# Optimization experiments

Measured on AMD Instinct MI355X. Metric: run time of the kernel, lower is better.

## Reference

```python
import jax, jax.numpy as jnp
import numpy as np

B, T, D_MODEL, N_HEADS = 2, 2048, 1024, 16
HS = D_MODEL // N_HEADS  # 64


def setup_inputs() -> dict:
    key = jax.random.key(0)
    k1, k2, k3 = jax.random.split(key, 3)
    x = jax.random.normal(k1, (B, T, D_MODEL), dtype=jnp.float32)
    # torch nn.Linear weights: (out_features, in_features)
    W_qkv = jax.random.normal(k2, (3 * D_MODEL, D_MODEL), dtype=jnp.float32) * (D_MODEL ** -0.5)
    W_out = jax.random.normal(k3, (D_MODEL, D_MODEL), dtype=jnp.float32) * (D_MODEL ** -0.5)
    return {"x": x, "W_qkv": W_qkv, "W_out": W_out}


def reference(x, W_qkv, W_out):
    Bx, Tx, Dm = x.shape
    nH, Hs = N_HEADS, HS
    # qkv projection: (B, T, 3*D) -> split heads -> (B, 3*nH, T, Hs) -> chunk
    qkv = x @ W_qkv.T
    qkv = qkv.reshape(Bx, Tx, 3 * nH, Hs).transpose(0, 2, 1, 3)  # B (3nH) T Hs
    q, k, v = qkv[:, :nH], qkv[:, nH:2 * nH], qkv[:, 2 * nH:]
    # q: softmax over head dim, scaled
    q = jax.nn.softmax(q, axis=-1) * (Hs ** -0.5)
    # causal linear attention via cumsum of outer products (non-loop branch)
    k_exp = jnp.exp(k - jnp.max(k, axis=2, keepdims=True))          # B nH T Hs
    k_exp_cumsum = jnp.cumsum(k_exp, axis=2)                        # B nH T Hs
    kv_outer = jnp.einsum('bhtc,bhtd->bhtcd', k_exp, v)             # B nH T Hs Hs
    kv_cumsum = jnp.cumsum(kv_outer, axis=2)                        # B nH T Hs Hs
    kv = kv_cumsum / (k_exp_cumsum[..., None] + 1e-9)
    xo = jnp.einsum('bhtc,bhtcd->bhtd', q, kv)                      # B nH T Hs
    # cat heads: B nH T Hs -> B T (nH Hs)
    xo = xo.transpose(0, 2, 1, 3).reshape(Bx, Tx, Dm)
    return xo @ W_out.T
```

## Files before the change

### kernel.cpp

```cpp
#include <hip/hip_runtime.h>

typedef __bf16 bf16;
typedef __bf16 bf16x8 __attribute__((ext_vector_type(8)));
typedef float  f32x4  __attribute__((ext_vector_type(4)));

#define MFMA16(a, b, c) __builtin_amdgcn_mfma_f32_16x16x32_bf16((a), (b), (c), 0, 0, 0)

#define GLOAD16(gp, lp) __builtin_amdgcn_global_load_lds( \
    (const __attribute__((address_space(1))) void*)(gp),  \
    (__attribute__((address_space(3))) void*)(lp), 16, 0, 0)

#define BAR __builtin_amdgcn_s_barrier()
#define WAITL do { asm volatile("s_waitcnt lgkmcnt(0)" ::: "memory"); \
                   __builtin_amdgcn_sched_barrier(0); } while (0)
#define WAITV6 asm volatile("s_waitcnt vmcnt(6)" ::: "memory")
#define WAITV0 asm volatile("s_waitcnt vmcnt(0)" ::: "memory")

__global__ __launch_bounds__(256) void cvt3_k(const float* __restrict__ x,
                                              const float* __restrict__ wq,
                                              const float* __restrict__ wo,
                                              bf16* __restrict__ xbf,
                                              bf16* __restrict__ wqkv,
                                              bf16* __restrict__ wout) {
    int i = blockIdx.x * 256 + threadIdx.x;
    const float* in; bf16* out; int off;
    if (i < 524288)       { in = x;  out = xbf;  off = i; }
    else if (i < 917504)  { in = wq; out = wqkv; off = i - 524288; }
    else                  { in = wo; out = wout; off = i - 917504; }
    f32x4 a = *(const f32x4*)(in + (size_t)off * 8);
    f32x4 b = *(const f32x4*)(in + (size_t)off * 8 + 4);
    bf16x8 o;
    o[0] = (bf16)a[0]; o[1] = (bf16)a[1]; o[2] = (bf16)a[2]; o[3] = (bf16)a[3];
    o[4] = (bf16)b[0]; o[5] = (bf16)b[1]; o[6] = (bf16)b[2]; o[7] = (bf16)b[3];
    *(bf16x8*)(out + (size_t)off * 8) = o;
}

template <typename CT>
__global__ __launch_bounds__(512, 2) void gemm256(const bf16* __restrict__ A,
                                                  const bf16* __restrict__ B,
                                                  CT* __restrict__ C,
                                                  int M, int N, int K) {
    __shared__ bf16 sA[2][256 * 64];
    __shared__ bf16 sB[2][256 * 64];
    const int tid = threadIdx.x, lane = tid & 63, w = tid >> 6;
    const int wm = w >> 2, wn = w & 3;

    const int nwg = gridDim.x * gridDim.y;
    const int lin = blockIdx.y * gridDim.x + blockIdx.x;
    const int cpx = nwg >> 3;
    const int swzb = (lin & 7) * cpx + (lin >> 3);
    const int row0 = (swzb / gridDim.x) * 256, col0 = (swzb % gridDim.x) * 256;
    const int nt = K >> 6;

    const int sw3   = (lane & 7) * 8;
    const int s0    = (lane >> 4) * 8;
    const int koff0 = s0 ^ sw3;
    const int koff1 = (s0 | 32) ^ sw3;
    const int aoff = (wm * 128 + (lane & 15)) * 64;
    const int boff = (wn * 64  + (lane & 15)) * 64;

    auto stgA = [&](int slot, int t, int i) {
        int c = i * 512 + tid;
        int r = c >> 3;
        int c8 = ((c & 7) * 8) ^ ((r & 7) * 8);
        GLOAD16(A + (size_t)(row0 + r) * K + t * 64 + c8, &sA[slot][c * 8]);
    };
    auto stgB = [&](int slot, int t, int i) {
        int c = i * 512 + tid;
        int r = c >> 3;
        int c8 = ((c & 7) * 8) ^ ((r & 7) * 8);
        GLOAD16(B + (size_t)(col0 + r) * K + t * 64 + c8, &sB[slot][c * 8]);
    };

    f32x4 acc[8][4] = {};

    #pragma unroll
    for (int i = 0; i < 4; ++i) stgA(0, 0, i);
    #pragma unroll
    for (int i = 0; i < 4; ++i) stgB(0, 0, i);
    #pragma unroll
    for (int i = 0; i < 4; ++i) stgA(1, 1, i);
    stgB(1, 1, 0); stgB(1, 1, 1);
    WAITV6;
    BAR;

    for (int j = 0; j < nt; ++j) {
        const int s = j & 1;
        const bf16* sa = sA[s];
        const bf16* sb = sB[s];
        bf16x8 a[4][2], b[4][2];

        #pragma unroll
        for (int mi = 0; mi < 4; ++mi) {
            a[mi][0] = *(const bf16x8*)&sa[aoff + mi * 1024 + koff0];
            a[mi][1] = *(const bf16x8*)&sa[aoff + mi * 1024 + koff1];
        }
        #pragma unroll
        for (int ni = 0; ni < 2; ++ni) {
            b[ni][0] = *(const bf16x8*)&sb[boff + ni * 1024 + koff0];
            b[ni][1] = *(const bf16x8*)&sb[boff + ni * 1024 + koff1];
        }
        if (j + 1 < nt) { stgB(s ^ 1, j + 1, 2); stgB(s ^ 1, j + 1, 3); }
        BAR; WAITL;
        __builtin_amdgcn_s_setprio(1);
        #pragma unroll
        for (int mi = 0; mi < 4; ++mi)
            #pragma unroll
            for (int ni = 0; ni < 2; ++ni) {
                acc[mi][ni] = MFMA16(a[mi][0], b[ni][0], acc[mi][ni]);
                acc[mi][ni] = MFMA16(a[mi][1], b[ni][1], acc[mi][ni]);
            }
        __builtin_amdgcn_s_setprio(0);
        BAR;

        #pragma unroll
        for (int ni = 2; ni < 4; ++ni) {
            b[ni][0] = *(const bf16x8*)&sb[boff + ni * 1024 + koff0];
            b[ni][1] = *(const bf16x8*)&sb[boff + ni * 1024 + koff1];
        }
        BAR; WAITL;
        __builtin_amdgcn_s_setprio(1);
        #pragma unroll
        for (int mi = 0; mi < 4; ++mi)
            #pragma unroll
            for (int ni = 2; ni < 4; ++ni) {
                acc[mi][ni] = MFMA16(a[mi][0], b[ni][0], acc[mi][ni]);
                acc[mi][ni] = MFMA16(a[mi][1], b[ni][1], acc[mi][ni]);
            }
        __builtin_amdgcn_s_setprio(0);
        BAR;

        #pragma unroll
        for (int mi = 0; mi < 4; ++mi) {
            a[mi][0] = *(const bf16x8*)&sa[aoff + (mi + 4) * 1024 + koff0];
            a[mi][1] = *(const bf16x8*)&sa[aoff + (mi + 4) * 1024 + koff1];
        }
        BAR; WAITL;
        __builtin_amdgcn_s_setprio(1);
        #pragma unroll
        for (int mi = 0; mi < 4; ++mi)
            #pragma unroll
            for (int ni = 0; ni < 2; ++ni) {
                acc[mi + 4][ni] = MFMA16(a[mi][0], b[ni][0], acc[mi + 4][ni]);
                acc[mi + 4][ni] = MFMA16(a[mi][1], b[ni][1], acc[mi + 4][ni]);
            }
        __builtin_amdgcn_s_setprio(0);
        BAR;

        if (j + 2 < nt) {
            #pragma unroll
            for (int i = 0; i < 4; ++i) stgA(s, j + 2, i);
            stgB(s, j + 2, 0); stgB(s, j + 2, 1);
            WAITV6;
        } else if (j + 1 < nt) {
            WAITV0;
        }
        BAR; WAITL;
        __builtin_amdgcn_s_setprio(1);
        #pragma unroll
        for (int mi = 0; mi < 4; ++mi)
            #pragma unroll
            for (int ni = 2; ni < 4; ++ni) {
                acc[mi + 4][ni] = MFMA16(a[mi][0], b[ni][0], acc[mi + 4][ni]);
                acc[mi + 4][ni] = MFMA16(a[mi][1], b[ni][1], acc[mi + 4][ni]);
            }
        __builtin_amdgcn_s_setprio(0);
        BAR;
    }

    const int crow = row0 + wm * 128 + (lane >> 4) * 4;
    const int ccol = col0 + wn * 64 + (lane & 15);
    #pragma unroll
    for (int mi = 0; mi < 8; ++mi)
        #pragma unroll
        for (int ni = 0; ni < 4; ++ni)
            #pragma unroll
            for (int r = 0; r < 4; ++r)
                C[(size_t)(crow + mi * 16 + r) * N + ccol + ni * 16] = (CT)acc[mi][ni][r];
}

template <typename CT>
__global__ __launch_bounds__(256) void gemm_nt(const bf16* __restrict__ A,
                                               const bf16* __restrict__ B,
                                               CT* __restrict__ C, int M, int N, int K) {
    __shared__ __align__(16) bf16 As[128 * 64];
    __shared__ __align__(16) bf16 Bs[128 * 64];
    const int tid  = threadIdx.x;
    const int lane = tid & 63;
    const int w    = tid >> 6;
    const int wm   = w >> 1, wn = w & 1;

    const int nwg = gridDim.x * gridDim.y;
    const int lin = blockIdx.y * gridDim.x + blockIdx.x;
    const int cpx = nwg >> 3;
    const int swzb = (lin & 7) * cpx + (lin >> 3);
    const int row0 = (swzb / gridDim.x) * 128, col0 = (swzb % gridDim.x) * 128;

    const int sr   = tid >> 3, sc = (tid & 7) * 8;
    const int sw3   = (lane & 7) * 8;
    const int s0    = (lane >> 4) * 8;
    const int kcs[2] = { s0 ^ sw3, (s0 | 32) ^ sw3 };

    f32x4 acc[4][4] = {};

    for (int k0 = 0; k0 < K; k0 += 64) {
        __syncthreads();
        #pragma unroll
        for (int i = 0; i < 4; ++i) {
            int r = sr + i * 32;
            int c8 = sc ^ ((r & 7) * 8);
            GLOAD16(A + (size_t)(row0 + r) * K + k0 + c8, &As[(i * 256 + tid) * 8]);
            GLOAD16(B + (size_t)(col0 + r) * K + k0 + c8, &Bs[(i * 256 + tid) * 8]);
        }
        __syncthreads();
        #pragma unroll
        for (int kk = 0; kk < 2; ++kk) {
            const int kc = kcs[kk];
            bf16x8 af[4], bfr[4];
            #pragma unroll
            for (int mi = 0; mi < 4; ++mi)
                af[mi] = *(const bf16x8*)&As[(wm * 64 + mi * 16 + (lane & 15)) * 64 + kc];
            #pragma unroll
            for (int ni = 0; ni < 4; ++ni)
                bfr[ni] = *(const bf16x8*)&Bs[(wn * 64 + ni * 16 + (lane & 15)) * 64 + kc];
            #pragma unroll
            for (int mi = 0; mi < 4; ++mi)
                #pragma unroll
                for (int ni = 0; ni < 4; ++ni)
                    acc[mi][ni] = MFMA16(af[mi], bfr[ni], acc[mi][ni]);
        }
    }
    const int crow = row0 + wm * 64 + (lane >> 4) * 4;
    const int ccol = col0 + wn * 64 + (lane & 15);
    #pragma unroll
    for (int mi = 0; mi < 4; ++mi)
        #pragma unroll
        for (int ni = 0; ni < 4; ++ni)
            #pragma unroll
            for (int r = 0; r < 4; ++r)
                C[(size_t)(crow + mi * 16 + r) * N + ccol + ni * 16] = (CT)acc[mi][ni][r];
}

__global__ __launch_bounds__(256) void qsoft_k(bf16* __restrict__ qkv) {
    int tg = blockIdx.x * 256 + threadIdx.x;
    int h = tg & 15, r = tg >> 4;
    bf16* q = qkv + (size_t)r * 3072 + h * 64;
    bf16x8 buf[8];
    float v[64];
    #pragma unroll
    for (int i = 0; i < 8; ++i) buf[i] = *(const bf16x8*)(q + i * 8);
    float m = -3.0e38f;
    #pragma unroll
    for (int i = 0; i < 8; ++i)
        #pragma unroll
        for (int e = 0; e < 8; ++e) { v[i * 8 + e] = (float)buf[i][e]; m = fmaxf(m, v[i * 8 + e]); }
    float s = 0.f;
    #pragma unroll
    for (int i = 0; i < 64; ++i) { v[i] = expf(v[i] - m); s += v[i]; }
    float inv = 0.125f / s;
    #pragma unroll
    for (int i = 0; i < 8; ++i) {
        bf16x8 o;
        #pragma unroll
        for (int e = 0; e < 8; ++e) o[e] = (bf16)(v[i * 8 + e] * inv);
        *(bf16x8*)(q + i * 8) = o;
    }
}

__global__ __launch_bounds__(64) void scanA_k(const bf16* __restrict__ qkv, float* __restrict__ part) {
    int blk = blockIdx.x;
    int bh = blk >> 5, seg = blk & 31;
    int b = bh >> 4, h = bh & 15;
    int c = threadIdx.x;
    const bf16* kb = qkv + (size_t)b * 2048 * 3072 + 1024 + h * 64 + c;
    float s = 0.f;
    for (int t0 = seg * 64; t0 < seg * 64 + 64; t0 += 8) {
        float e[8];
        #pragma unroll
        for (int u = 0; u < 8; ++u) e[u] = (float)kb[(size_t)(t0 + u) * 3072];
        #pragma unroll
        for (int u = 0; u < 8; ++u) s += expf(e[u]);
    }
    part[blk * 64 + c] = s;
}

__global__ __launch_bounds__(64) void scanB_k(bf16* __restrict__ qkv, const float* __restrict__ part) {
    int blk = blockIdx.x;
    int bh = blk >> 5, seg = blk & 31;
    int b = bh >> 4, h = bh & 15;
    int c = threadIdx.x;
    bf16* qb = qkv + (size_t)b * 2048 * 3072 + h * 64 + c;
    bf16* kb = qb + 1024;
    float run = 0.f;
    for (int i = 0; i < seg; ++i) run += part[(bh * 32 + i) * 64 + c];
    for (int t0 = seg * 64; t0 < seg * 64 + 64; t0 += 8) {
        float e[8], qv[8];
        #pragma unroll
        for (int u = 0; u < 8; ++u) e[u] = (float)kb[(size_t)(t0 + u) * 3072];
        #pragma unroll
        for (int u = 0; u < 8; ++u) qv[u] = (float)qb[(size_t)(t0 + u) * 3072];
        #pragma unroll
        for (int u = 0; u < 8; ++u) {
            e[u] = expf(e[u]);
            run += e[u];
            qv[u] = qv[u] / (run + 1e-9f);
        }
        #pragma unroll
        for (int u = 0; u < 8; ++u) {
            qb[(size_t)(t0 + u) * 3072] = (bf16)qv[u];
            kb[(size_t)(t0 + u) * 3072] = (bf16)e[u];
        }
    }
}

__global__ __launch_bounds__(256) void kvchunk_k(const bf16* __restrict__ qkv, float* __restrict__ Wc) {
    __shared__ bf16 KT[64][136];
    __shared__ bf16 VT[64][136];
    const int blk = blockIdx.x, bh = blk >> 4, j = blk & 15;
    const int b = bh >> 4, h = bh & 15;
    const int tid = threadIdx.x, lane = tid & 63, w = tid >> 6;
    const bf16* kbase = qkv + (size_t)(b * 2048 + j * 128) * 3072 + 1024 + h * 64;
    const bf16* vbase = kbase + 1024;

    #pragma unroll
    for (int i = 0; i < 4; ++i) {
        int idx = i * 256 + tid;
        int s = idx >> 3, cg = (idx & 7) * 8;
        bf16x8 k8 = *(const bf16x8*)(kbase + (size_t)s * 3072 + cg);
        bf16x8 v8 = *(const bf16x8*)(vbase + (size_t)s * 3072 + cg);
        #pragma unroll
        for (int e = 0; e < 8; ++e) {
            int d = cg + e;
            int sw2 = s ^ (((d >> 3) & 7) << 3);
            KT[d][sw2] = k8[e];
            VT[d][sw2] = v8[e];
        }
    }
    __syncthreads();

    f32x4 acc[4] = {};
    const int dr = w * 16 + (lane & 15);
    const int swd = ((dr >> 3) & 7) << 3;
    #pragma unroll
    for (int ks = 0; ks < 4; ++ks) {
        const int sc = ks * 32 + (lane >> 4) * 8;
        bf16x8 av = *(const bf16x8*)&VT[dr][sc ^ swd];
        #pragma unroll
        for (int ni = 0; ni < 4; ++ni) {
            int cr = ni * 16 + (lane & 15);
            bf16x8 bk = *(const bf16x8*)&KT[cr][sc ^ (((cr >> 3) & 7) << 3)];
            acc[ni] = MFMA16(av, bk, acc[ni]);
        }
    }
    float* out = Wc + (size_t)blk * 4096;
    const int dw = w * 16 + (lane >> 4) * 4;
    #pragma unroll
    for (int ni = 0; ni < 4; ++ni)
        #pragma unroll
        for (int r = 0; r < 4; ++r)
            out[(dw + r) * 64 + ni * 16 + (lane & 15)] = acc[ni][r];
}

__global__ __launch_bounds__(256) void kvscan_k(const float* __restrict__ Wc, bf16* __restrict__ Wpre) {
    int e = blockIdx.x * 256 + threadIdx.x;
    int bh = e >> 12, off = e & 4095;
    float run = 0.f;
    #pragma unroll
    for (int j = 0; j < 16; ++j) {
        size_t idx = (size_t)(bh * 16 + j) * 4096 + off;
        Wpre[idx] = (bf16)run;
        run += Wc[idx];
    }
}

__global__ __launch_bounds__(256) void attn2_k(const bf16* __restrict__ qkv,
                                               const bf16* __restrict__ Wpre,
                                               bf16* __restrict__ xo) {
    __shared__ bf16 Ks[128][72];
    __shared__ bf16 VTs[64][136];
    __shared__ bf16 Ss[128][136];
    const int bh = blockIdx.y, b = bh >> 4, h = bh & 15;
    const int ti = blockIdx.x, t0 = ti * 128;
    const int tid = threadIdx.x, lane = tid & 63, w = tid >> 6;
    const bf16* qn = qkv + (size_t)b * 2048 * 3072 + h * 64;
    const bf16* ke = qn + 1024;
    const bf16* vv = qn + 2048;

    bf16x8 qf[2][2];
    #pragma unroll
    for (int mi = 0; mi < 2; ++mi)
        #pragma unroll
        for (int kk = 0; kk < 2; ++kk)
            qf[mi][kk] = *(const bf16x8*)(qn + (size_t)(t0 + w * 32 + mi * 16 + (lane & 15)) * 3072
                                          + kk * 32 + (lane >> 4) * 8);
    const bf16* wp = Wpre + (size_t)(bh * 16 + ti) * 4096;
    bf16x8 wf[4][2];
    #pragma unroll
    for (int ni = 0; ni < 4; ++ni)
        #pragma unroll
        for (int kk = 0; kk < 2; ++kk)
            wf[ni][kk] = *(const bf16x8*)(wp + (ni * 16 + (lane & 15)) * 64 + kk * 32 + (lane >> 4) * 8);

    #pragma unroll
    for (int i = 0; i < 4; ++i) {
        int idx = i * 256 + tid;
        int s = idx >> 3, cg = (idx & 7) * 8;
        *(f32x4*)&Ks[s][cg] = *(const f32x4*)(ke + (size_t)(t0 + s) * 3072 + cg);
        bf16x8 v8 = *(const bf16x8*)(vv + (size_t)(t0 + s) * 3072 + cg);
        #pragma unroll
        for (int e = 0; e < 8; ++e) {
            int d = cg + e;
            VTs[d][s ^ (((d >> 3) & 7) << 3)] = v8[e];
        }
    }
    __syncthreads();

    f32x4 accO[2][4] = {};
    #pragma unroll
    for (int kk = 0; kk < 2; ++kk)
        #pragma unroll
        for (int mi = 0; mi < 2; ++mi)
            #pragma unroll
            for (int ni = 0; ni < 4; ++ni)
                accO[mi][ni] = MFMA16(qf[mi][kk], wf[ni][kk], accO[mi][ni]);

    f32x4 accS[2][8] = {};
    #pragma unroll
    for (int kk = 0; kk < 2; ++kk) {
        const int kc = kk * 32 + (lane >> 4) * 8;
        bf16x8 kf[8];
        #pragma unroll
        for (int ni = 0; ni < 8; ++ni) kf[ni] = *(const bf16x8*)&Ks[ni * 16 + (lane & 15)][kc];
        #pragma unroll
        for (int mi = 0; mi < 2; ++mi)
            #pragma unroll
            for (int ni = 0; ni < 8; ++ni)
                accS[mi][ni] = MFMA16(qf[mi][kk], kf[ni], accS[mi][ni]);
    }
    #pragma unroll
    for (int mi = 0; mi < 2; ++mi)
        #pragma unroll
        for (int ni = 0; ni < 8; ++ni) {
            const int tb = w * 32 + mi * 16 + (lane >> 4) * 4;
            const int sb = ni * 16 + (lane & 15);
            #pragma unroll
            for (int r = 0; r < 4; ++r) {
                float sv = accS[mi][ni][r];
                if (sb > tb + r) sv = 0.f;
                Ss[tb + r][sb] = (bf16)sv;
            }
        }
    __syncthreads();

    #pragma unroll
    for (int ks = 0; ks < 4; ++ks) {
        const int kc = ks * 32 + (lane >> 4) * 8;
        bf16x8 sf[2], vf[4];
        #pragma unroll
        for (int mi = 0; mi < 2; ++mi) sf[mi] = *(const bf16x8*)&Ss[w * 32 + mi * 16 + (lane & 15)][kc];
        #pragma unroll
        for (int ni = 0; ni < 4; ++ni) {
            int d = ni * 16 + (lane & 15);
            vf[ni] = *(const bf16x8*)&VTs[d][kc ^ (((d >> 3) & 7) << 3)];
        }
        #pragma unroll
        for (int mi = 0; mi < 2; ++mi)
            #pragma unroll
            for (int ni = 0; ni < 4; ++ni)
                accO[mi][ni] = MFMA16(sf[mi], vf[ni], accO[mi][ni]);
    }

    #pragma unroll
    for (int mi = 0; mi < 2; ++mi)
        #pragma unroll
        for (int ni = 0; ni < 4; ++ni) {
            const int trow = t0 + w * 32 + mi * 16 + (lane >> 4) * 4;
            const int d = ni * 16 + (lane & 15);
            #pragma unroll
            for (int r = 0; r < 4; ++r)
                xo[(size_t)(b * 2048 + trow + r) * 1024 + h * 64 + d] = (bf16)accO[mi][ni][r];
        }
}

extern "C" void kernel_launch(void* const* d_in, const int* in_sizes, int n_in,
                              void* d_out, int out_size, void* d_ws, size_t ws_size,
                              hipStream_t stream) {
    const float* x  = (const float*)d_in[0];
    const float* wq = (const float*)d_in[1];
    const float* wo = (const float*)d_in[2];

    char* ws = (char*)d_ws;
    bf16*  xbf  = (bf16*)(ws);
    float* Wc   = (float*)(ws);
    bf16*  xo   = (bf16*)(ws);
    bf16*  wqkv = (bf16*)(ws + (8u << 20));
    bf16*  Wpre = (bf16*)(ws + (8u << 20));
    bf16*  wout = (bf16*)(ws + (14u << 20));
    bf16*  qkv  = (bf16*)(ws + (16u << 20));
    float* part = (float*)(ws + (40u << 20));

    cvt3_k<<<4096, 256, 0, stream>>>(x, wq, wo, xbf, wqkv, wout);

    gemm256<bf16><<<dim3(12, 16), 512, 0, stream>>>(xbf, wqkv, qkv, 4096, 3072, 1024);

    qsoft_k<<<256, 256, 0, stream>>>(qkv);
    scanA_k<<<1024, 64, 0, stream>>>(qkv, part);
    scanB_k<<<1024, 64, 0, stream>>>(qkv, part);

    kvchunk_k<<<512, 256, 0, stream>>>(qkv, Wc);
    kvscan_k<<<512, 256, 0, stream>>>(Wc, Wpre);
    attn2_k<<<dim3(16, 32), 256, 0, stream>>>(qkv, Wpre, xo);

    gemm_nt<float><<<dim3(8, 32), 256, 0, stream>>>(xo, wout, (float*)d_out, 4096, 1024, 1024);
}
```

Baseline: 124.7 us.

## Software-pipeline LDS fragment loads in GEMM and merge q-softmax with k-exp scan

```diff
diff --git a/kernel.cpp b/kernel.cpp
--- a/kernel.cpp
+++ b/kernel.cpp
@@ -11,10 +11,236 @@
     (__attribute__((address_space(3))) void*)(lp), 16, 0, 0)
 
 #define BAR __builtin_amdgcn_s_barrier()
-#define WAITL do { asm volatile("s_waitcnt lgkmcnt(0)" ::: "memory"); \
-                   __builtin_amdgcn_sched_barrier(0); } while (0)
-#define WAITV6 asm volatile("s_waitcnt vmcnt(6)" ::: "memory")
+#define WAITV8 asm volatile("s_waitcnt vmcnt(8)" ::: "memory")
 #define WAITV0 asm volatile("s_waitcnt vmcnt(0)" ::: "memory")
+
+template <typename CT>
+__global__ __launch_bounds__(512, 2) void gemm256(const bf16* __restrict__ A,
+                                                  const bf16* __restrict__ B,
+                                                  CT* __restrict__ C,
+                                                  int M, int N, int K) {
+    __shared__ bf16 sA[2][256 * 64];
+    __shared__ bf16 sB[2][256 * 64];
+    const int tid = threadIdx.x, lane = tid & 63, w = tid >> 6;
+    const int wm = w >> 2, wn = w & 3;
+
+    const int nwg = gridDim.x * gridDim.y;
+    const int lin = blockIdx.y * gridDim.x + blockIdx.x;
+    const int cpx = nwg >> 3;
+    const int swzb = (lin & 7) * cpx + (lin >> 3);
+    const int row0 = (swzb / gridDim.x) * 256, col0 = (swzb % gridDim.x) * 256;
+    const int nt = K >> 6;
+
+    const int sw3   = (lane & 7) * 8;
+    const int s0    = (lane >> 4) * 8;
+    const int koff0 = s0 ^ sw3;
+    const int koff1 = (s0 | 32) ^ sw3;
+    const int aoff = (wm * 128 + (lane & 15)) * 64;
+    const int boff = (wn * 64  + (lane & 15)) * 64;
+
+    auto stgA = [&](int slot, int t, int i) {
+        int c = i * 512 + tid;
+        int r = c >> 3;
+        int c8 = ((c & 7) * 8) ^ ((r & 7) * 8);
+        GLOAD16(A + (size_t)(row0 + r) * K + t * 64 + c8, &sA[slot][c * 8]);
+    };
+    auto stgB = [&](int slot, int t, int i) {
+        int c = i * 512 + tid;
+        int r = c >> 3;
+        int c8 = ((c & 7) * 8) ^ ((r & 7) * 8);
+        GLOAD16(B + (size_t)(col0 + r) * K + t * 64 + c8, &sB[slot][c * 8]);
+    };
+
+    f32x4 acc[8][4] = {};
+    bf16x8 a[4][2], b[2][2], a2[4][2], b2[2][2];
+
+    #pragma unroll
+    for (int i = 0; i < 4; ++i) stgA(0, 0, i);
+    #pragma unroll
+    for (int i = 0; i < 4; ++i) stgB(0, 0, i);
+    #pragma unroll
+    for (int i = 0; i < 4; ++i) stgA(1, 1, i);
+    #pragma unroll
+    for (int i = 0; i < 4; ++i) stgB(1, 1, i);
+    WAITV8;
+    BAR;
+    {
+        const bf16* sa = sA[0];
+        const bf16* sb = sB[0];
+        #pragma unroll
+        for (int mi = 0; mi < 4; ++mi) {
+            a[mi][0] = *(const bf16x8*)&sa[aoff + mi * 1024 + koff0];
+            a[mi][1] = *(const bf16x8*)&sa[aoff + mi * 1024 + koff1];
+        }
+        #pragma unroll
+        for (int ni = 0; ni < 2; ++ni) {
+            b[ni][0] = *(const bf16x8*)&sb[boff + ni * 1024 + koff0];
+            b[ni][1] = *(const bf16x8*)&sb[boff + ni * 1024 + koff1];
+        }
+    }
+
+    for (int j = 0; j < nt; ++j) {
+        const int s = j & 1;
+        const bf16* sa = sA[s];
+        const bf16* sb = sB[s];
+        const bf16* san = sA[s ^ 1];
+        const bf16* sbn = sB[s ^ 1];
+
+        #pragma unroll
+        for (int ni = 0; ni < 2; ++ni) {
+            b2[ni][0] = *(const bf16x8*)&sb[boff + (ni + 2) * 1024 + koff0];
+            b2[ni][1] = *(const bf16x8*)&sb[boff + (ni + 2) * 1024 + koff1];
+        }
+        BAR;
+        __builtin_amdgcn_s_setprio(1);
+        #pragma unroll
+        for (int mi = 0; mi < 4; ++mi)
+            #pragma unroll
+            for (int ni = 0; ni < 2; ++ni) {
+                acc[mi][ni] = MFMA16(a[mi][0], b[ni][0], acc[mi][ni]);
+                acc[mi][ni] = MFMA16(a[mi][1], b[ni][1], acc[mi][ni]);
+            }
+        __builtin_amdgcn_s_setprio(0);
+        BAR;
+
+        #pragma unroll
+        for (int mi = 0; mi < 4; ++mi) {
+            a2[mi][0] = *(const bf16x8*)&sa[aoff + (mi + 4) * 1024 + koff0];
+            a2[mi][1] = *(const bf16x8*)&sa[aoff + (mi + 4) * 1024 + koff1];
+        }
+        BAR;
+        __builtin_amdgcn_s_setprio(1);
+        #pragma unroll
+        for (int mi = 0; mi < 4; ++mi)
+            #pragma unroll
+            for (int ni = 0; ni < 2; ++ni) {
+                acc[mi][ni + 2] = MFMA16(a[mi][0], b2[ni][0], acc[mi][ni + 2]);
+                acc[mi][ni + 2] = MFMA16(a[mi][1], b2[ni][1], acc[mi][ni + 2]);
+            }
+        __builtin_amdgcn_s_setprio(0);
+        BAR;
+
+        if (j + 2 < nt) {
+            #pragma unroll
+            for (int i = 0; i < 4; ++i) stgB(s, j + 2, i);
+        }
+        BAR;
+        __builtin_amdgcn_s_setprio(1);
+        #pragma unroll
+        for (int mi = 0; mi < 4; ++mi)
+            #pragma unroll
+            for (int ni = 0; ni < 2; ++ni) {
+                acc[mi + 4][ni] = MFMA16(a2[mi][0], b[ni][0], acc[mi + 4][ni]);
+                acc[mi + 4][ni] = MFMA16(a2[mi][1], b[ni][1], acc[mi + 4][ni]);
+            }
+        __builtin_amdgcn_s_setprio(0);
+        BAR;
+
+        if (j + 2 < nt) {
+            #pragma unroll
+            for (int i = 0; i < 4; ++i) stgA(s, j + 2, i);
+            WAITV8;
+        } else if (j + 1 < nt) {
+            WAITV0;
+        }
+        BAR;
+        if (j + 1 < nt) {
+            #pragma unroll
+            for (int mi = 0; mi < 4; ++mi) {
+                a[mi][0] = *(const bf16x8*)&san[aoff + mi * 1024 + koff0];
+                a[mi][1] = *(const bf16x8*)&san[aoff + mi * 1024 + koff1];
+            }
+            #pragma unroll
+            for (int ni = 0; ni < 2; ++ni) {
+                b[ni][0] = *(const bf16x8*)&sbn[boff + ni * 1024 + koff0];
+                b[ni][1] = *(const bf16x8*)&sbn[boff + ni * 1024 + koff1];
+            }
+            __builtin_amdgcn_sched_barrier(0);
+        }
+        __builtin_amdgcn_s_setprio(1);
+        #pragma unroll
+        for (int mi = 0; mi < 4; ++mi)
+            #pragma unroll
+            for (int ni = 0; ni < 2; ++ni) {
+                acc[mi + 4][ni + 2] = MFMA16(a2[mi][0], b2[ni][0], acc[mi + 4][ni + 2]);
+                acc[mi + 4][ni + 2] = MFMA16(a2[mi][1], b2[ni][1], acc[mi + 4][ni + 2]);
+            }
+        __builtin_amdgcn_s_setprio(0);
+        BAR;
+    }
+
+    const int crow = row0 + wm * 128 + (lane >> 4) * 4;
+    const int ccol = col0 + wn * 64 + (lane & 15);
+    #pragma unroll
+    for (int mi = 0; mi < 8; ++mi)
+        #pragma unroll
+        for (int ni = 0; ni < 4; ++ni)
+            #pragma unroll
+            for (int r = 0; r < 4; ++r)
+                C[(size_t)(crow + mi * 16 + r) * N + ccol + ni * 16] = (CT)acc[mi][ni][r];
+}
+
+template <typename CT>
+__global__ __launch_bounds__(256) void gemm_nt(const bf16* __restrict__ A,
+                                               const bf16* __restrict__ B,
+                                               CT* __restrict__ C, int M, int N, int K) {
+    __shared__ __align__(16) bf16 As[128 * 64];
+    __shared__ __align__(16) bf16 Bs[128 * 64];
+    const int tid  = threadIdx.x;
+    const int lane = tid & 63;
+    const int w    = tid >> 6;
+    const int wm   = w >> 1, wn = w & 1;
+
+    const int nwg = gridDim.x * gridDim.y;
+    const int lin = blockIdx.y * gridDim.x + blockIdx.x;
+    const int cpx = nwg >> 3;
+    const int swzb = (lin & 7) * cpx + (lin >> 3);
+    const int row0 = (swzb / gridDim.x) * 128, col0 = (swzb % gridDim.x) * 128;
+
+    const int sr   = tid >> 3, sc = (tid & 7) * 8;
+    const int sw3   = (lane & 7) * 8;
+    const int s0    = (lane >> 4) * 8;
+    const int kcs[2] = { s0 ^ sw3, (s0 | 32) ^ sw3 };
+
+    f32x4 acc[4][4] = {};
+
+    for (int k0 = 0; k0 < K; k0 += 64) {
+        __syncthreads();
+        #pragma unroll
+        for (int i = 0; i < 4; ++i) {
+            int r = sr + i * 32;
+            int c8 = sc ^ ((r & 7) * 8);
+            GLOAD16(A + (size_t)(row0 + r) * K + k0 + c8, &As[(i * 256 + tid) * 8]);
+            GLOAD16(B + (size_t)(col0 + r) * K + k0 + c8, &Bs[(i * 256 + tid) * 8]);
+        }
+        __syncthreads();
+        #pragma unroll
+        for (int kk = 0; kk < 2; ++kk) {
+            const int kc = kcs[kk];
+            bf16x8 af[4], bfr[4];
+            #pragma unroll
+            for (int mi = 0; mi < 4; ++mi)
+                af[mi] = *(const bf16x8*)&As[(wm * 64 + mi * 16 + (lane & 15)) * 64 + kc];
+            #pragma unroll
+            for (int ni = 0; ni < 4; ++ni)
+                bfr[ni] = *(const bf16x8*)&Bs[(wn * 64 + ni * 16 + (lane & 15)) * 64 + kc];
+            #pragma unroll
+            for (int mi = 0; mi < 4; ++mi)
+                #pragma unroll
+                for (int ni = 0; ni < 4; ++ni)
+                    acc[mi][ni] = MFMA16(af[mi], bfr[ni], acc[mi][ni]);
+        }
+    }
+    const int crow = row0 + wm * 64 + (lane >> 4) * 4;
+    const int ccol = col0 + wn * 64 + (lane & 15);
+    #pragma unroll
+    for (int mi = 0; mi < 4; ++mi)
+        #pragma unroll
+        for (int ni = 0; ni < 4; ++ni)
+            #pragma unroll
+            for (int r = 0; r < 4; ++r)
+                C[(size_t)(crow + mi * 16 + r) * N + ccol + ni * 16] = (CT)acc[mi][ni][r];
+}
 
 __global__ __launch_bounds__(256) void cvt3_k(const float* __restrict__ x,
                                               const float* __restrict__ wq,
@@ -35,253 +261,47 @@
     *(bf16x8*)(out + (size_t)off * 8) = o;
 }
 
-template <typename CT>
-__global__ __launch_bounds__(512, 2) void gemm256(const bf16* __restrict__ A,
-                                                  const bf16* __restrict__ B,
-                                                  CT* __restrict__ C,
-                                                  int M, int N, int K) {
-    __shared__ bf16 sA[2][256 * 64];
-    __shared__ bf16 sB[2][256 * 64];
-    const int tid = threadIdx.x, lane = tid & 63, w = tid >> 6;
-    const int wm = w >> 2, wn = w & 3;
-
-    const int nwg = gridDim.x * gridDim.y;
-    const int lin = blockIdx.y * gridDim.x + blockIdx.x;
-    const int cpx = nwg >> 3;
-    const int swzb = (lin & 7) * cpx + (lin >> 3);
-    const int row0 = (swzb / gridDim.x) * 256, col0 = (swzb % gridDim.x) * 256;
-    const int nt = K >> 6;
-
-    const int sw3   = (lane & 7) * 8;
-    const int s0    = (lane >> 4) * 8;
-    const int koff0 = s0 ^ sw3;
-    const int koff1 = (s0 | 32) ^ sw3;
-    const int aoff = (wm * 128 + (lane & 15)) * 64;
-    const int boff = (wn * 64  + (lane & 15)) * 64;
-
-    auto stgA = [&](int slot, int t, int i) {
-        int c = i * 512 + tid;
-        int r = c >> 3;
-        int c8 = ((c & 7) * 8) ^ ((r & 7) * 8);
-        GLOAD16(A + (size_t)(row0 + r) * K + t * 64 + c8, &sA[slot][c * 8]);
-    };
-    auto stgB = [&](int slot, int t, int i) {
-        int c = i * 512 + tid;
-        int r = c >> 3;
-        int c8 = ((c & 7) * 8) ^ ((r & 7) * 8);
-        GLOAD16(B + (size_t)(col0 + r) * K + t * 64 + c8, &sB[slot][c * 8]);
-    };
-
-    f32x4 acc[8][4] = {};
-
-    #pragma unroll
-    for (int i = 0; i < 4; ++i) stgA(0, 0, i);
-    #pragma unroll
-    for (int i = 0; i < 4; ++i) stgB(0, 0, i);
-    #pragma unroll
-    for (int i = 0; i < 4; ++i) stgA(1, 1, i);
-    stgB(1, 1, 0); stgB(1, 1, 1);
-    WAITV6;
-    BAR;
-
-    for (int j = 0; j < nt; ++j) {
-        const int s = j & 1;
-        const bf16* sa = sA[s];
-        const bf16* sb = sB[s];
-        bf16x8 a[4][2], b[4][2];
-
-        #pragma unroll
-        for (int mi = 0; mi < 4; ++mi) {
-            a[mi][0] = *(const bf16x8*)&sa[aoff + mi * 1024 + koff0];
-            a[mi][1] = *(const bf16x8*)&sa[aoff + mi * 1024 + koff1];
-        }
-        #pragma unroll
-        for (int ni = 0; ni < 2; ++ni) {
-            b[ni][0] = *(const bf16x8*)&sb[boff + ni * 1024 + koff0];
-            b[ni][1] = *(const bf16x8*)&sb[boff + ni * 1024 + koff1];
-        }
-        if (j + 1 < nt) { stgB(s ^ 1, j + 1, 2); stgB(s ^ 1, j + 1, 3); }
-        BAR; WAITL;
-        __builtin_amdgcn_s_setprio(1);
-        #pragma unroll
-        for (int mi = 0; mi < 4; ++mi)
-            #pragma unroll
-            for (int ni = 0; ni < 2; ++ni) {
-                acc[mi][ni] = MFMA16(a[mi][0], b[ni][0], acc[mi][ni]);
-                acc[mi][ni] = MFMA16(a[mi][1], b[ni][1], acc[mi][ni]);
-            }
-        __builtin_amdgcn_s_setprio(0);
-        BAR;
-
-        #pragma unroll
-        for (int ni = 2; ni < 4; ++ni) {
-            b[ni][0] = *(const bf16x8*)&sb[boff + ni * 1024 + koff0];
-            b[ni][1] = *(const bf16x8*)&sb[boff + ni * 1024 + koff1];
-        }
-        BAR; WAITL;
-        __builtin_amdgcn_s_setprio(1);
-        #pragma unroll
-        for (int mi = 0; mi < 4; ++mi)
-            #pragma unroll
-            for (int ni = 2; ni < 4; ++ni) {
-                acc[mi][ni] = MFMA16(a[mi][0], b[ni][0], acc[mi][ni]);
-                acc[mi][ni] = MFMA16(a[mi][1], b[ni][1], acc[mi][ni]);
-            }
-        __builtin_amdgcn_s_setprio(0);
-        BAR;
-
-        #pragma unroll
-        for (int mi = 0; mi < 4; ++mi) {
-            a[mi][0] = *(const bf16x8*)&sa[aoff + (mi + 4) * 1024 + koff0];
-            a[mi][1] = *(const bf16x8*)&sa[aoff + (mi + 4) * 1024 + koff1];
-        }
-        BAR; WAITL;
-        __builtin_amdgcn_s_setprio(1);
-        #pragma unroll
-        for (int mi = 0; mi < 4; ++mi)
-            #pragma unroll
-            for (int ni = 0; ni < 2; ++ni) {
-                acc[mi + 4][ni] = MFMA16(a[mi][0], b[ni][0], acc[mi + 4][ni]);
-                acc[mi + 4][ni] = MFMA16(a[mi][1], b[ni][1], acc[mi + 4][ni]);
-            }
-        __builtin_amdgcn_s_setprio(0);
-        BAR;
-
-        if (j + 2 < nt) {
-            #pragma unroll
-            for (int i = 0; i < 4; ++i) stgA(s, j + 2, i);
-            stgB(s, j + 2, 0); stgB(s, j + 2, 1);
-            WAITV6;
-        } else if (j + 1 < nt) {
-            WAITV0;
-        }
-        BAR; WAITL;
-        __builtin_amdgcn_s_setprio(1);
-        #pragma unroll
-        for (int mi = 0; mi < 4; ++mi)
-            #pragma unroll
-            for (int ni = 2; ni < 4; ++ni) {
-                acc[mi + 4][ni] = MFMA16(a[mi][0], b[ni][0], acc[mi + 4][ni]);
-                acc[mi + 4][ni] = MFMA16(a[mi][1], b[ni][1], acc[mi + 4][ni]);
-            }
-        __builtin_amdgcn_s_setprio(0);
-        BAR;
-    }
-
-    const int crow = row0 + wm * 128 + (lane >> 4) * 4;
-    const int ccol = col0 + wn * 64 + (lane & 15);
-    #pragma unroll
-    for (int mi = 0; mi < 8; ++mi)
-        #pragma unroll
-        for (int ni = 0; ni < 4; ++ni)
-            #pragma unroll
-            for (int r = 0; r < 4; ++r)
-                C[(size_t)(crow + mi * 16 + r) * N + ccol + ni * 16] = (CT)acc[mi][ni][r];
-}
-
-template <typename CT>
-__global__ __launch_bounds__(256) void gemm_nt(const bf16* __restrict__ A,
-                                               const bf16* __restrict__ B,
-                                               CT* __restrict__ C, int M, int N, int K) {
-    __shared__ __align__(16) bf16 As[128 * 64];
-    __shared__ __align__(16) bf16 Bs[128 * 64];
-    const int tid  = threadIdx.x;
-    const int lane = tid & 63;
-    const int w    = tid >> 6;
-    const int wm   = w >> 1, wn = w & 1;
-
-    const int nwg = gridDim.x * gridDim.y;
-    const int lin = blockIdx.y * gridDim.x + blockIdx.x;
-    const int cpx = nwg >> 3;
-    const int swzb = (lin & 7) * cpx + (lin >> 3);
-    const int row0 = (swzb / gridDim.x) * 128, col0 = (swzb % gridDim.x) * 128;
-
-    const int sr   = tid >> 3, sc = (tid & 7) * 8;
-    const int sw3   = (lane & 7) * 8;
-    const int s0    = (lane >> 4) * 8;
-    const int kcs[2] = { s0 ^ sw3, (s0 | 32) ^ sw3 };
-
-    f32x4 acc[4][4] = {};
-
-    for (int k0 = 0; k0 < K; k0 += 64) {
-        __syncthreads();
-        #pragma unroll
-        for (int i = 0; i < 4; ++i) {
-            int r = sr + i * 32;
-            int c8 = sc ^ ((r & 7) * 8);
-            GLOAD16(A + (size_t)(row0 + r) * K + k0 + c8, &As[(i * 256 + tid) * 8]);
-            GLOAD16(B + (size_t)(col0 + r) * K + k0 + c8, &Bs[(i * 256 + tid) * 8]);
-        }
-        __syncthreads();
-        #pragma unroll
-        for (int kk = 0; kk < 2; ++kk) {
-            const int kc = kcs[kk];
-            bf16x8 af[4], bfr[4];
-            #pragma unroll
-            for (int mi = 0; mi < 4; ++mi)
-                af[mi] = *(const bf16x8*)&As[(wm * 64 + mi * 16 + (lane & 15)) * 64 + kc];
-            #pragma unroll
-            for (int ni = 0; ni < 4; ++ni)
-                bfr[ni] = *(const bf16x8*)&Bs[(wn * 64 + ni * 16 + (lane & 15)) * 64 + kc];
-            #pragma unroll
-            for (int mi = 0; mi < 4; ++mi)
-                #pragma unroll
-                for (int ni = 0; ni < 4; ++ni)
-                    acc[mi][ni] = MFMA16(af[mi], bfr[ni], acc[mi][ni]);
-        }
-    }
-    const int crow = row0 + wm * 64 + (lane >> 4) * 4;
-    const int ccol = col0 + wn * 64 + (lane & 15);
-    #pragma unroll
-    for (int mi = 0; mi < 4; ++mi)
-        #pragma unroll
-        for (int ni = 0; ni < 4; ++ni)
-            #pragma unroll
-            for (int r = 0; r < 4; ++r)
-                C[(size_t)(crow + mi * 16 + r) * N + ccol + ni * 16] = (CT)acc[mi][ni][r];
-}
-
-__global__ __launch_bounds__(256) void qsoft_k(bf16* __restrict__ qkv) {
-    int tg = blockIdx.x * 256 + threadIdx.x;
-    int h = tg & 15, r = tg >> 4;
-    bf16* q = qkv + (size_t)r * 3072 + h * 64;
-    bf16x8 buf[8];
-    float v[64];
-    #pragma unroll
-    for (int i = 0; i < 8; ++i) buf[i] = *(const bf16x8*)(q + i * 8);
-    float m = -3.0e38f;
-    #pragma unroll
-    for (int i = 0; i < 8; ++i)
-        #pragma unroll
-        for (int e = 0; e < 8; ++e) { v[i * 8 + e] = (float)buf[i][e]; m = fmaxf(m, v[i * 8 + e]); }
-    float s = 0.f;
-    #pragma unroll
-    for (int i = 0; i < 64; ++i) { v[i] = expf(v[i] - m); s += v[i]; }
-    float inv = 0.125f / s;
-    #pragma unroll
-    for (int i = 0; i < 8; ++i) {
-        bf16x8 o;
-        #pragma unroll
-        for (int e = 0; e < 8; ++e) o[e] = (bf16)(v[i * 8 + e] * inv);
-        *(bf16x8*)(q + i * 8) = o;
-    }
-}
-
-__global__ __launch_bounds__(64) void scanA_k(const bf16* __restrict__ qkv, float* __restrict__ part) {
-    int blk = blockIdx.x;
-    int bh = blk >> 5, seg = blk & 31;
-    int b = bh >> 4, h = bh & 15;
-    int c = threadIdx.x;
-    const bf16* kb = qkv + (size_t)b * 2048 * 3072 + 1024 + h * 64 + c;
-    float s = 0.f;
-    for (int t0 = seg * 64; t0 < seg * 64 + 64; t0 += 8) {
-        float e[8];
-        #pragma unroll
-        for (int u = 0; u < 8; ++u) e[u] = (float)kb[(size_t)(t0 + u) * 3072];
-        #pragma unroll
-        for (int u = 0; u < 8; ++u) s += expf(e[u]);
-    }
-    part[blk * 64 + c] = s;
+__global__ __launch_bounds__(256) void qsA_k(bf16* __restrict__ qkv, float* __restrict__ part) {
+    if (blockIdx.x < 256) {
+        int tg = blockIdx.x * 256 + threadIdx.x;
+        int h = tg & 15, r = tg >> 4;
+        bf16* q = qkv + (size_t)r * 3072 + h * 64;
+        bf16x8 buf[8];
+        float v[64];
+        #pragma unroll
+        for (int i = 0; i < 8; ++i) buf[i] = *(const bf16x8*)(q + i * 8);
+        float m = -3.0e38f;
+        #pragma unroll
+        for (int i = 0; i < 8; ++i)
+            #pragma unroll
+            for (int e = 0; e < 8; ++e) { v[i * 8 + e] = (float)buf[i][e]; m = fmaxf(m, v[i * 8 + e]); }
+        float s = 0.f;
+        #pragma unroll
+        for (int i = 0; i < 64; ++i) { v[i] = expf(v[i] - m); s += v[i]; }
+        float inv = 0.125f / s;
+        #pragma unroll
+        for (int i = 0; i < 8; ++i) {
+            bf16x8 o;
+            #pragma unroll
+            for (int e = 0; e < 8; ++e) o[e] = (bf16)(v[i * 8 + e] * inv);
+            *(bf16x8*)(q + i * 8) = o;
+        }
+    } else {
+        int blk = (blockIdx.x - 256) * 4 + (threadIdx.x >> 6);
+        int bh = blk >> 5, seg = blk & 31;
+        int b = bh >> 4, h = bh & 15;
+        int c = threadIdx.x & 63;
+        const bf16* kb = qkv + (size_t)b * 2048 * 3072 + 1024 + h * 64 + c;
+        float s = 0.f;
+        for (int t0 = seg * 64; t0 < seg * 64 + 64; t0 += 8) {
+            float e[8];
+            #pragma unroll
+            for (int u = 0; u < 8; ++u) e[u] = (float)kb[(size_t)(t0 + u) * 3072];
+            #pragma unroll
+            for (int u = 0; u < 8; ++u) s += expf(e[u]);
+        }
+        part[blk * 64 + c] = s;
+    }
 }
 
 __global__ __launch_bounds__(64) void scanB_k(bf16* __restrict__ qkv, const float* __restrict__ part) {
@@ -503,8 +523,7 @@
 
     gemm256<bf16><<<dim3(12, 16), 512, 0, stream>>>(xbf, wqkv, qkv, 4096, 3072, 1024);
 
-    qsoft_k<<<256, 256, 0, stream>>>(qkv);
-    scanA_k<<<1024, 64, 0, stream>>>(qkv, part);
+    qsA_k<<<512, 256, 0, stream>>>(qkv, part);
     scanB_k<<<1024, 64, 0, stream>>>(qkv, part);
 
     kvchunk_k<<<512, 256, 0, stream>>>(qkv, Wc);
```

After: 125.4 us. Within noise of the previous version (+0.6%).
